# Kernel optimization log

Measured on AMD Instinct MI355X. Metric: run time of the kernel, lower is better.

The kernel has to match this reference:

```python
import jax, jax.numpy as jnp
import numpy as np

B, N, E = 8, 10000, 160000
T_IN, T_OUT, C_IN, C_OUT, HID = 12, 12, 2, 2, 128
FLAT = C_IN * T_IN  # 24
EPS = 1e-5  # BatchNorm1d default eps


def setup_inputs() -> dict:
    key = jax.random.key(0)
    ks = jax.random.split(key, 16)
    s = 0.05
    return {
        "x": jax.random.normal(ks[0], (B, T_IN, N, C_IN), jnp.float32),
        "edge_index": jax.random.randint(ks[1], (2, E), 0, N, dtype=jnp.int64),
        "Wl0": jax.random.normal(ks[2], (FLAT, HID), jnp.float32) * s,
        "Wr0": jax.random.normal(ks[3], (FLAT, HID), jnp.float32) * s,
        "bl0": jax.random.normal(ks[4], (HID,), jnp.float32) * s,
        "Wl12": jax.random.normal(ks[5], (2, HID, HID), jnp.float32) * s,
        "Wr12": jax.random.normal(ks[6], (2, HID, HID), jnp.float32) * s,
        "bl12": jax.random.normal(ks[7], (2, HID), jnp.float32) * s,
        "bn_g": jax.random.uniform(ks[8], (3, HID), jnp.float32, 0.5, 1.5),
        "bn_b": jax.random.normal(ks[9], (3, HID), jnp.float32) * s,
        "bn_m": jax.random.normal(ks[10], (3, HID), jnp.float32) * s,
        "bn_v": jax.random.uniform(ks[11], (3, HID), jnp.float32, 0.5, 1.5),
        "head_W": jax.random.normal(ks[12], (HID, T_OUT * C_OUT), jnp.float32) * s,
        "head_b": jax.random.normal(ks[13], (T_OUT * C_OUT,), jnp.float32) * s,
    }


def _sage_conv(h, src, dst, inv_deg, Wl, Wr, bl):
    # PyG SAGEConv (mean aggr): out = lin_l(mean_{j->i} x_j) + lin_r(x_i)
    msg = h[:, src, :]                                   # [B, E, F] gather
    agg = jnp.zeros_like(h).at[:, dst, :].add(msg)       # scatter-add
    mean = agg * inv_deg[None, :, None]                  # mean over neighbors
    return mean @ Wl + bl + h @ Wr


def reference(x, edge_index, Wl0, Wr0, bl0, Wl12, Wr12, bl12,
              bn_g, bn_b, bn_m, bn_v, head_W, head_b):
    src, dst = edge_index[0], edge_index[1]
    deg = jnp.zeros((N,), x.dtype).at[dst].add(1.0)
    inv_deg = 1.0 / jnp.maximum(deg, 1.0)

    # (B, T, N, C) -> (B, N, T*C)
    h = x.transpose(0, 2, 1, 3).reshape(B, N, FLAT)

    layers = [(Wl0, Wr0, bl0), (Wl12[0], Wr12[0], bl12[0]), (Wl12[1], Wr12[1], bl12[1])]
    for i, (Wl, Wr, bl) in enumerate(layers):
        h = _sage_conv(h, src, dst, inv_deg, Wl, Wr, bl)
        # BatchNorm1d in eval mode (running stats); Dropout is identity in eval
        h = (h - bn_m[i]) * (bn_g[i] / jnp.sqrt(bn_v[i] + EPS)) + bn_b[i]
        h = jax.nn.relu(h)

    out = h @ head_W + head_b                            # [B, N, T_out*C_out]
    out = out.reshape(B, N, T_OUT, C_OUT).transpose(0, 2, 1, 3)
    return out                                           # [B, T_out, N, C_out]
```

## Files before the change

kernel.cpp:

```cpp
#include <hip/hip_runtime.h>

#define NB 8
#define NNODE 10000
#define NEDGE 160000
#define MROWS 80000
#define TIN 12
#define EPSBN 1e-5f

typedef __attribute__((ext_vector_type(8))) short bf16x8;
typedef __attribute__((ext_vector_type(4))) float f32x4;
typedef unsigned short u16;
typedef unsigned int u32;

static __device__ __forceinline__ u16 f2bf(float f) {
    unsigned int u = __builtin_bit_cast(unsigned int, f);
    u = (u + 0x7fffu + ((u >> 16) & 1u)) >> 16;
    return (u16)u;
}
static __device__ __forceinline__ float bf2f(u16 h) {
    unsigned int u = ((unsigned int)h) << 16;
    return __builtin_bit_cast(float, u);
}

__global__ __launch_bounds__(256) void fused_pre(const float* __restrict__ x,
                                                 u16* __restrict__ X0,
                                                 const int* __restrict__ ei,
                                                 int* __restrict__ degi,
                                                 const float* __restrict__ Wl0,
                                                 const float* __restrict__ Wr0,
                                                 const float* __restrict__ bl0,
                                                 const float* __restrict__ Wl12,
                                                 const float* __restrict__ Wr12,
                                                 const float* __restrict__ bl12,
                                                 const float* __restrict__ g,
                                                 const float* __restrict__ bb,
                                                 const float* __restrict__ m,
                                                 const float* __restrict__ v,
                                                 u16* __restrict__ W0T, u16* __restrict__ W1T,
                                                 u16* __restrict__ W2T,
                                                 float* __restrict__ bias012) {
    int blk = blockIdx.x;
    if (blk < 3750) {
        int id = blk * 256 + threadIdx.x;
        if (id >= NB * TIN * NNODE) return;
        int n = id % NNODE;
        int bt = id / NNODE;
        int b = bt / TIN, tt = bt % TIN;
        float2 vv = *(const float2*)&x[(size_t)id * 2];
        u32 packed = (u32)f2bf(vv.x) | ((u32)f2bf(vv.y) << 16);
        *(u32*)&X0[(n * NB + b) * 64 + 24 + tt * 2] = packed;
    } else if (blk < 4375) {
        int e = (blk - 3750) * 256 + threadIdx.x;
        if (e < NEDGE) atomicAdd(&degi[ei[NEDGE + e]], 1);
    } else {
        int c = blk - 4375, k = threadIdx.x;
        float s0 = g[c] / sqrtf(v[c] + EPSBN);
        float s1 = g[128 + c] / sqrtf(v[128 + c] + EPSBN);
        float s2 = g[256 + c] / sqrtf(v[256 + c] + EPSBN);
        if (k < 64) {
            float val = (k < 24) ? Wl0[k * 128 + c] : ((k < 48) ? Wr0[(k - 24) * 128 + c] : 0.0f);
            W0T[c * 64 + k] = f2bf(val * s0);
        }
        float v1 = (k < 128) ? Wl12[k * 128 + c] : Wr12[(k - 128) * 128 + c];
        W1T[c * 256 + k] = f2bf(v1 * s1);
        float v2 = (k < 128) ? Wl12[128 * 128 + k * 128 + c]
                             : Wr12[128 * 128 + (k - 128) * 128 + c];
        W2T[c * 256 + k] = f2bf(v2 * s2);
        if (k < 3) {
            float sl = g[k * 128 + c] / sqrtf(v[k * 128 + c] + EPSBN);
            float blv = (k == 0) ? bl0[c] : bl12[(k - 1) * 128 + c];
            bias012[k * 128 + c] = blv * sl + bb[k * 128 + c] - m[k * 128 + c] * sl;
        }
    }
}

__global__ __launch_bounds__(1024) void scan_kernel(const int* __restrict__ degi,
                                                    int* __restrict__ row_ptr,
                                                    float* __restrict__ inv_deg,
                                                    int* __restrict__ cursor) {
    __shared__ int sdata[1024];
    const int t = threadIdx.x;
    const int CH = 10;
    const int i0 = t * CH;
    int sum = 0;
    for (int i = i0; i < i0 + CH && i < NNODE; ++i) sum += degi[i];
    sdata[t] = sum;
    for (int off = 1; off < 1024; off <<= 1) {
        __syncthreads();
        int vv = (t >= off) ? sdata[t - off] : 0;
        __syncthreads();
        sdata[t] += vv;
    }
    __syncthreads();
    int run = sdata[t] - sum;
    for (int i = i0; i < i0 + CH && i < NNODE; ++i) {
        row_ptr[i] = run;
        int d = degi[i];
        run += d;
        inv_deg[i] = 1.0f / (float)max(d, 1);
        cursor[i] = 0;
    }
    if (t == 1023) row_ptr[NNODE] = sdata[1023];
}

__global__ void csr_fill(const int* __restrict__ ei, const int* __restrict__ row_ptr,
                         int* __restrict__ cursor, int* __restrict__ csr_src) {
    int e = blockIdx.x * blockDim.x + threadIdx.x;
    if (e < NEDGE) {
        int d = ei[NEDGE + e];
        int pos = atomicAdd(&cursor[d], 1);
        csr_src[row_ptr[d] + pos] = ei[e];
    }
}

__global__ __launch_bounds__(192) void agg24(u16* __restrict__ X0,
                                             const int* __restrict__ rp,
                                             const int* __restrict__ cs,
                                             const float* __restrict__ inv) {
    int u = threadIdx.x;
    int n = blockIdx.x * 2 + (u / 96);
    int w = u % 96;
    int b = w / 12, cp = w % 12;
    int p0 = rp[n], p1 = rp[n + 1];
    float a0 = 0, a1 = 0, b0 = 0, b1 = 0, c0 = 0, c1 = 0, d0 = 0, d1 = 0;
    int p = p0;
    for (; p + 4 <= p1; p += 4) {
        int s0 = cs[p], s1 = cs[p + 1], s2 = cs[p + 2], s3 = cs[p + 3];
        u32 v0 = *(const u32*)&X0[(s0 * NB + b) * 64 + 24 + cp * 2];
        u32 v1 = *(const u32*)&X0[(s1 * NB + b) * 64 + 24 + cp * 2];
        u32 v2 = *(const u32*)&X0[(s2 * NB + b) * 64 + 24 + cp * 2];
        u32 v3 = *(const u32*)&X0[(s3 * NB + b) * 64 + 24 + cp * 2];
        a0 += bf2f((u16)(v0 & 0xffff)); a1 += bf2f((u16)(v0 >> 16));
        b0 += bf2f((u16)(v1 & 0xffff)); b1 += bf2f((u16)(v1 >> 16));
        c0 += bf2f((u16)(v2 & 0xffff)); c1 += bf2f((u16)(v2 >> 16));
        d0 += bf2f((u16)(v3 & 0xffff)); d1 += bf2f((u16)(v3 >> 16));
    }
    for (; p < p1; ++p) {
        int s = cs[p];
        u32 vv = *(const u32*)&X0[(s * NB + b) * 64 + 24 + cp * 2];
        a0 += bf2f((u16)(vv & 0xffff)); a1 += bf2f((u16)(vv >> 16));
    }
    float sc = inv[n];
    float r0 = (a0 + b0) + (c0 + d0), r1 = (a1 + b1) + (c1 + d1);
    u32 o = (u32)f2bf(r0 * sc) | ((u32)f2bf(r1 * sc) << 16);
    *(u32*)&X0[(n * NB + b) * 64 + cp * 2] = o;
}

__global__ __launch_bounds__(64) void agg128c(u16* __restrict__ X,
                                              const int* __restrict__ rp,
                                              const int* __restrict__ cs,
                                              const float* __restrict__ inv) {
    int bid = blockIdx.x;
    int c = bid & 7;
    int n = bid >> 3;
    int t = threadIdx.x;
    int b = t >> 3, q = t & 7;
    int p0 = rp[n], p1 = rp[n + 1];
    const u16* hb = X + ((size_t)(8 + c) * MROWS) * 16;
    float a0 = 0, a1 = 0, b0 = 0, b1 = 0, c0 = 0, c1 = 0, d0 = 0, d1 = 0;
    int p = p0;
    for (; p + 4 <= p1; p += 4) {
        int s0 = cs[p], s1 = cs[p + 1], s2 = cs[p + 2], s3 = cs[p + 3];
        u32 v0 = *(const u32*)&hb[(s0 * NB + b) * 16 + q * 2];
        u32 v1 = *(const u32*)&hb[(s1 * NB + b) * 16 + q * 2];
        u32 v2 = *(const u32*)&hb[(s2 * NB + b) * 16 + q * 2];
        u32 v3 = *(const u32*)&hb[(s3 * NB + b) * 16 + q * 2];
        a0 += bf2f((u16)(v0 & 0xffff)); a1 += bf2f((u16)(v0 >> 16));
        b0 += bf2f((u16)(v1 & 0xffff)); b1 += bf2f((u16)(v1 >> 16));
        c0 += bf2f((u16)(v2 & 0xffff)); c1 += bf2f((u16)(v2 >> 16));
        d0 += bf2f((u16)(v3 & 0xffff)); d1 += bf2f((u16)(v3 >> 16));
    }
    for (; p < p1; ++p) {
        int s = cs[p];
        u32 vv = *(const u32*)&hb[(s * NB + b) * 16 + q * 2];
        a0 += bf2f((u16)(vv & 0xffff)); a1 += bf2f((u16)(vv >> 16));
    }
    float sc = inv[n];
    float r0 = (a0 + b0) + (c0 + d0), r1 = (a1 + b1) + (c1 + d1);
    u32 o = (u32)f2bf(r0 * sc) | ((u32)f2bf(r1 * sc) << 16);
    *(u32*)&X[((size_t)c * MROWS + n * NB + b) * 16 + q * 2] = o;
}

#define LOADA(dst, stp) { \
    const int k0_ = (stp) * 32 + kg * 8; \
    _Pragma("unroll") \
    for (int m_ = 0; m_ < 4; ++m_) { \
        const int row_ = rowbase + m_ * 16; \
        const u16* ap_; \
        if (INC) ap_ = A + ((size_t)(k0_ >> 4) * MROWS + row_) * 16 + (k0_ & 15); \
        else     ap_ = A + (size_t)row_ * K + k0_; \
        dst[m_] = *(const bf16x8*)ap_; \
    } }

#define MFMAS(av, stp) { \
    const int k0_ = (stp) * 32 + kg * 8; \
    bf16x8 bv_[4]; \
    _Pragma("unroll") \
    for (int n_ = 0; n_ < 4; ++n_) \
        bv_[n_] = *(const bf16x8*)&Bs[wc * 64 + n_ * 16 + r16][k0_]; \
    _Pragma("unroll") \
    for (int m_ = 0; m_ < 4; ++m_) \
        _Pragma("unroll") \
        for (int n_ = 0; n_ < 4; ++n_) \
            acc[m_][n_] = __builtin_amdgcn_mfma_f32_16x16x32_bf16(av[m_], bv_[n_], acc[m_][n_], 0, 0, 0); }

template<int K, bool INC, bool OUTC>
__global__ __launch_bounds__(640) void gemm_mfma(const u16* __restrict__ A,
                                                 const u16* __restrict__ WT,
                                                 const float* __restrict__ bias,
                                                 u16* __restrict__ out) {
    constexpr int NSTEP = K / 32;
    __shared__ __align__(16) short Bs[128][K + 8];
    const int t = threadIdx.x;
    const int row0 = blockIdx.x * 320;
    const int lane = t & 63, wid = t >> 6;
    const int wr = wid >> 1, wc = wid & 1;
    const int r16 = lane & 15, kg = lane >> 4;

    if (t < 512) {
        const int col = t >> 2, k0 = (t & 3) * (K / 4);
        #pragma unroll
        for (int j = 0; j < K / 32; ++j)
            *(bf16x8*)&Bs[col][k0 + j * 8] =
                *(const bf16x8*)&WT[col * K + k0 + j * 8];
    }
    __syncthreads();

    f32x4 acc[4][4];
    #pragma unroll
    for (int m = 0; m < 4; ++m)
        #pragma unroll
        for (int n = 0; n < 4; ++n)
            acc[m][n] = (f32x4){0.f, 0.f, 0.f, 0.f};

    const int rowbase = row0 + wr * 64 + r16;

    bf16x8 avA[4], avB[4];
    LOADA(avA, 0)
    #pragma unroll
    for (int s2 = 0; s2 < NSTEP; s2 += 2) {
        if (s2 + 1 < NSTEP) LOADA(avB, s2 + 1)
        MFMAS(avA, s2)
        if (s2 + 2 < NSTEP) LOADA(avA, s2 + 2)
        if (s2 + 1 < NSTEP) MFMAS(avB, s2 + 1)
    }

    #pragma unroll
    for (int m = 0; m < 4; ++m) {
        #pragma unroll
        for (int n = 0; n < 4; ++n) {
            int col = wc * 64 + n * 16 + r16;
            float bvf = bias[col];
            #pragma unroll
            for (int r = 0; r < 4; ++r) {
                int grow = row0 + wr * 64 + m * 16 + kg * 4 + r;
                float val = fmaxf(acc[m][n][r] + bvf, 0.0f);
                u16 h = f2bf(val);
                if (OUTC)
                    out[((size_t)(8 + wc * 4 + n) * MROWS + grow) * 16 + r16] = h;
                else
                    out[(size_t)grow * 128 + col] = h;
            }
        }
    }
}

__global__ __launch_bounds__(256) void head_kernel(const u16* __restrict__ H3,
                                                   const float* __restrict__ hW,
                                                   const float* __restrict__ hb,
                                                   float* __restrict__ out) {
    __shared__ float Ws[128 * 24];
    __shared__ float bs[24];
    int t = threadIdx.x;
    for (int i = t; i < 128 * 24; i += 256) Ws[i] = hW[i];
    if (t < 24) bs[t] = hb[t];
    __syncthreads();
    int row = blockIdx.x * 256 + t;
    if (row >= MROWS) return;
    float acc[24];
    #pragma unroll
    for (int c = 0; c < 24; ++c) acc[c] = bs[c];
    const u16* a = &H3[(size_t)row * 128];
    for (int kq = 0; kq < 16; ++kq) {
        bf16x8 raw = *(const bf16x8*)&a[kq * 8];
        #pragma unroll
        for (int j = 0; j < 8; ++j) {
            float av = bf2f((u16)raw[j]);
            #pragma unroll
            for (int c = 0; c < 24; ++c)
                acc[c] = fmaf(av, Ws[(kq * 8 + j) * 24 + c], acc[c]);
        }
    }
    int n = row >> 3, b = row & 7;
    #pragma unroll
    for (int tt = 0; tt < 12; ++tt) {
        float2 o;
        o.x = acc[tt * 2 + 0];
        o.y = acc[tt * 2 + 1];
        *(float2*)&out[((b * TIN + tt) * NNODE + n) * 2] = o;
    }
}

extern "C" void kernel_launch(void* const* d_in, const int* in_sizes, int n_in,
                              void* d_out, int out_size, void* d_ws, size_t ws_size,
                              hipStream_t stream) {
    const float* x      = (const float*)d_in[0];
    const int*   ei     = (const int*)d_in[1];
    const float* Wl0    = (const float*)d_in[2];
    const float* Wr0    = (const float*)d_in[3];
    const float* bl0    = (const float*)d_in[4];
    const float* Wl12   = (const float*)d_in[5];
    const float* Wr12   = (const float*)d_in[6];
    const float* bl12   = (const float*)d_in[7];
    const float* bn_g   = (const float*)d_in[8];
    const float* bn_b   = (const float*)d_in[9];
    const float* bn_m   = (const float*)d_in[10];
    const float* bn_v   = (const float*)d_in[11];
    const float* headW  = (const float*)d_in[12];
    const float* headb  = (const float*)d_in[13];
    float* out = (float*)d_out;

    u16* X0 = (u16*)d_ws;
    u16* X1 = X0 + (size_t)MROWS * 64;
    u16* X2 = X1 + (size_t)MROWS * 256;
    u16* W0T = X2 + (size_t)MROWS * 256;
    u16* W1T = W0T + 128 * 64;
    u16* W2T = W1T + 128 * 256;
    float* bias012 = (float*)(W2T + 128 * 256);
    float* inv_deg = bias012 + 3 * 128;
    int* degi    = (int*)(inv_deg + NNODE);
    int* row_ptr = degi + NNODE;
    int* cursor  = row_ptr + (NNODE + 1);
    int* csr_src = cursor + NNODE;
    u16* H3 = X1;

    hipMemsetAsync(degi, 0, sizeof(int) * NNODE, stream);

    fused_pre<<<4503, 256, 0, stream>>>(x, X0, ei, degi, Wl0, Wr0, bl0, Wl12, Wr12,
                                        bl12, bn_g, bn_b, bn_m, bn_v,
                                        W0T, W1T, W2T, bias012);
    scan_kernel<<<1, 1024, 0, stream>>>(degi, row_ptr, inv_deg, cursor);
    csr_fill<<<(NEDGE + 255) / 256, 256, 0, stream>>>(ei, row_ptr, cursor, csr_src);

    agg24<<<NNODE / 2, 192, 0, stream>>>(X0, row_ptr, csr_src, inv_deg);
    gemm_mfma<64, false, true><<<250, 640, 0, stream>>>(X0, W0T, bias012, X1);
    agg128c<<<NNODE * 8, 64, 0, stream>>>(X1, row_ptr, csr_src, inv_deg);
    gemm_mfma<256, true, true><<<250, 640, 0, stream>>>(X1, W1T, bias012 + 128, X2);
    agg128c<<<NNODE * 8, 64, 0, stream>>>(X2, row_ptr, csr_src, inv_deg);
    gemm_mfma<256, true, false><<<250, 640, 0, stream>>>(X2, W2T, bias012 + 256, H3);
    head_kernel<<<(MROWS + 255) / 256, 256, 0, stream>>>(H3, headW, headb, out);
}
```

Before: 283.1 us.

## Fuse output head into last SAGE GEMM and shrink X0 row stride

The separate head kernel is folded into the epilogue of the third MFMA GEMM. The post-ReLU tile is staged in shared memory and each pair of threads computes 12 of the 24 head outputs per row, so the H3 intermediate is no longer written to and re-read from global memory, and one launch disappears. The first-layer buffer X0 now uses a 48-element row stride instead of 64. The input transpose now has one thread per row, packing all 12 timesteps into vector stores. The GEMM still reads K=64 with the smaller stride, so it relies on zero weight padding and a small tail pad past the last row. The fused epilogue also needs much more shared memory.

```diff
diff --git a/kernel.cpp b/kernel.cpp
--- a/kernel.cpp
+++ b/kernel.cpp
@@ -40,20 +40,25 @@
                                                  u16* __restrict__ W2T,
                                                  float* __restrict__ bias012) {
     int blk = blockIdx.x;
-    if (blk < 3750) {
-        int id = blk * 256 + threadIdx.x;
-        if (id >= NB * TIN * NNODE) return;
-        int n = id % NNODE;
-        int bt = id / NNODE;
-        int b = bt / TIN, tt = bt % TIN;
-        float2 vv = *(const float2*)&x[(size_t)id * 2];
-        u32 packed = (u32)f2bf(vv.x) | ((u32)f2bf(vv.y) << 16);
-        *(u32*)&X0[(n * NB + b) * 64 + 24 + tt * 2] = packed;
-    } else if (blk < 4375) {
-        int e = (blk - 3750) * 256 + threadIdx.x;
+    if (blk < 313) {
+        int row = blk * 256 + threadIdx.x;
+        if (row >= MROWS) return;
+        int n = row >> 3, b = row & 7;
+        u32 w[12];
+        #pragma unroll
+        for (int tt = 0; tt < 12; ++tt) {
+            float2 vv = *(const float2*)&x[(size_t)((b * 12 + tt) * NNODE + n) * 2];
+            w[tt] = (u32)f2bf(vv.x) | ((u32)f2bf(vv.y) << 16);
+        }
+        u32* dst = (u32*)&X0[(size_t)row * 48 + 24];
+        *(uint4*)(dst + 0) = make_uint4(w[0], w[1], w[2], w[3]);
+        *(uint4*)(dst + 4) = make_uint4(w[4], w[5], w[6], w[7]);
+        *(uint4*)(dst + 8) = make_uint4(w[8], w[9], w[10], w[11]);
+    } else if (blk < 938) {
+        int e = (blk - 313) * 256 + threadIdx.x;
         if (e < NEDGE) atomicAdd(&degi[ei[NEDGE + e]], 1);
     } else {
-        int c = blk - 4375, k = threadIdx.x;
+        int c = blk - 938, k = threadIdx.x;
         float s0 = g[c] / sqrtf(v[c] + EPSBN);
         float s1 = g[128 + c] / sqrtf(v[128 + c] + EPSBN);
         float s2 = g[256 + c] / sqrtf(v[256 + c] + EPSBN);
@@ -126,10 +131,10 @@
     int p = p0;
     for (; p + 4 <= p1; p += 4) {
         int s0 = cs[p], s1 = cs[p + 1], s2 = cs[p + 2], s3 = cs[p + 3];
-        u32 v0 = *(const u32*)&X0[(s0 * NB + b) * 64 + 24 + cp * 2];
-        u32 v1 = *(const u32*)&X0[(s1 * NB + b) * 64 + 24 + cp * 2];
-        u32 v2 = *(const u32*)&X0[(s2 * NB + b) * 64 + 24 + cp * 2];
-        u32 v3 = *(const u32*)&X0[(s3 * NB + b) * 64 + 24 + cp * 2];
+        u32 v0 = *(const u32*)&X0[(s0 * NB + b) * 48 + 24 + cp * 2];
+        u32 v1 = *(const u32*)&X0[(s1 * NB + b) * 48 + 24 + cp * 2];
+        u32 v2 = *(const u32*)&X0[(s2 * NB + b) * 48 + 24 + cp * 2];
+        u32 v3 = *(const u32*)&X0[(s3 * NB + b) * 48 + 24 + cp * 2];
         a0 += bf2f((u16)(v0 & 0xffff)); a1 += bf2f((u16)(v0 >> 16));
         b0 += bf2f((u16)(v1 & 0xffff)); b1 += bf2f((u16)(v1 >> 16));
         c0 += bf2f((u16)(v2 & 0xffff)); c1 += bf2f((u16)(v2 >> 16));
@@ -137,13 +142,13 @@
     }
     for (; p < p1; ++p) {
         int s = cs[p];
-        u32 vv = *(const u32*)&X0[(s * NB + b) * 64 + 24 + cp * 2];
+        u32 vv = *(const u32*)&X0[(s * NB + b) * 48 + 24 + cp * 2];
         a0 += bf2f((u16)(vv & 0xffff)); a1 += bf2f((u16)(vv >> 16));
     }
     float sc = inv[n];
     float r0 = (a0 + b0) + (c0 + d0), r1 = (a1 + b1) + (c1 + d1);
     u32 o = (u32)f2bf(r0 * sc) | ((u32)f2bf(r1 * sc) << 16);
-    *(u32*)&X0[(n * NB + b) * 64 + cp * 2] = o;
+    *(u32*)&X0[(n * NB + b) * 48 + cp * 2] = o;
 }
 
 __global__ __launch_bounds__(64) void agg128c(u16* __restrict__ X,
@@ -188,7 +193,7 @@
         const int row_ = rowbase + m_ * 16; \
         const u16* ap_; \
         if (INC) ap_ = A + ((size_t)(k0_ >> 4) * MROWS + row_) * 16 + (k0_ & 15); \
-        else     ap_ = A + (size_t)row_ * K + k0_; \
+        else     ap_ = A + (size_t)row_ * LDA + k0_; \
         dst[m_] = *(const bf16x8*)ap_; \
     } }
 
@@ -204,19 +209,34 @@
         for (int n_ = 0; n_ < 4; ++n_) \
             acc[m_][n_] = __builtin_amdgcn_mfma_f32_16x16x32_bf16(av[m_], bv_[n_], acc[m_][n_], 0, 0, 0); }
 
-template<int K, bool INC, bool OUTC>
+template<int K, int LDA, bool INC, bool HEAD>
 __global__ __launch_bounds__(640) void gemm_mfma(const u16* __restrict__ A,
                                                  const u16* __restrict__ WT,
                                                  const float* __restrict__ bias,
-                                                 u16* __restrict__ out) {
+                                                 const float* __restrict__ hW,
+                                                 const float* __restrict__ hb,
+                                                 u16* __restrict__ outc,
+                                                 float* __restrict__ outf) {
     constexpr int NSTEP = K / 32;
-    __shared__ __align__(16) short Bs[128][K + 8];
+    constexpr int BS_BYTES = 128 * (K + 8) * 2;
+    constexpr int HS_BYTES = 320 * 132 * 2;
+    constexpr int SMEM_BYTES = HEAD ? (HS_BYTES + 128 * 24 * 4 + 128) : BS_BYTES;
+    __shared__ __align__(16) char smem[SMEM_BYTES];
+    typedef short (*BsT)[K + 8];
+    BsT Bs = (BsT)smem;
+
     const int t = threadIdx.x;
     const int row0 = blockIdx.x * 320;
     const int lane = t & 63, wid = t >> 6;
     const int wr = wid >> 1, wc = wid & 1;
     const int r16 = lane & 15, kg = lane >> 4;
 
+    float* Wsf = (float*)(smem + HS_BYTES);
+    float* bsh = Wsf + 128 * 24;
+    if (HEAD) {
+        for (int i = t; i < 128 * 24; i += 640) Wsf[i] = hW[i];
+        if (t < 24) bsh[t] = hb[t];
+    }
     if (t < 512) {
         const int col = t >> 2, k0 = (t & 3) * (K / 4);
         #pragma unroll
@@ -245,59 +265,64 @@
         if (s2 + 1 < NSTEP) MFMAS(avB, s2 + 1)
     }
 
-    #pragma unroll
-    for (int m = 0; m < 4; ++m) {
-        #pragma unroll
-        for (int n = 0; n < 4; ++n) {
-            int col = wc * 64 + n * 16 + r16;
-            float bvf = bias[col];
+    if (!HEAD) {
+        #pragma unroll
+        for (int m = 0; m < 4; ++m)
             #pragma unroll
-            for (int r = 0; r < 4; ++r) {
-                int grow = row0 + wr * 64 + m * 16 + kg * 4 + r;
-                float val = fmaxf(acc[m][n][r] + bvf, 0.0f);
-                u16 h = f2bf(val);
-                if (OUTC)
-                    out[((size_t)(8 + wc * 4 + n) * MROWS + grow) * 16 + r16] = h;
-                else
-                    out[(size_t)grow * 128 + col] = h;
+            for (int n = 0; n < 4; ++n) {
+                int col = wc * 64 + n * 16 + r16;
+                float bvf = bias[col];
+                #pragma unroll
+                for (int r = 0; r < 4; ++r) {
+                    int grow = row0 + wr * 64 + m * 16 + kg * 4 + r;
+                    float val = fmaxf(acc[m][n][r] + bvf, 0.0f);
+                    outc[((size_t)(8 + wc * 4 + n) * MROWS + grow) * 16 + r16] = f2bf(val);
+                }
             }
-        }
-    }
-}
-
-__global__ __launch_bounds__(256) void head_kernel(const u16* __restrict__ H3,
-                                                   const float* __restrict__ hW,
-                                                   const float* __restrict__ hb,
-                                                   float* __restrict__ out) {
-    __shared__ float Ws[128 * 24];
-    __shared__ float bs[24];
-    int t = threadIdx.x;
-    for (int i = t; i < 128 * 24; i += 256) Ws[i] = hW[i];
-    if (t < 24) bs[t] = hb[t];
-    __syncthreads();
-    int row = blockIdx.x * 256 + t;
-    if (row >= MROWS) return;
-    float acc[24];
-    #pragma unroll
-    for (int c = 0; c < 24; ++c) acc[c] = bs[c];
-    const u16* a = &H3[(size_t)row * 128];
-    for (int kq = 0; kq < 16; ++kq) {
-        bf16x8 raw = *(const bf16x8*)&a[kq * 8];
-        #pragma unroll
-        for (int j = 0; j < 8; ++j) {
-            float av = bf2f((u16)raw[j]);
+    } else {
+        __syncthreads();
+        u16* Hs = (u16*)smem;
+        #pragma unroll
+        for (int m = 0; m < 4; ++m)
             #pragma unroll
-            for (int c = 0; c < 24; ++c)
-                acc[c] = fmaf(av, Ws[(kq * 8 + j) * 24 + c], acc[c]);
-        }
-    }
-    int n = row >> 3, b = row & 7;
-    #pragma unroll
-    for (int tt = 0; tt < 12; ++tt) {
-        float2 o;
-        o.x = acc[tt * 2 + 0];
-        o.y = acc[tt * 2 + 1];
-        *(float2*)&out[((b * TIN + tt) * NNODE + n) * 2] = o;
+            for (int n = 0; n < 4; ++n) {
+                int col = wc * 64 + n * 16 + r16;
+                float bvf = bias[col];
+                #pragma unroll
+                for (int r = 0; r < 4; ++r) {
+                    int lrow = wr * 64 + m * 16 + kg * 4 + r;
+                    Hs[lrow * 132 + col] = f2bf(fmaxf(acc[m][n][r] + bvf, 0.0f));
+                }
+            }
+        __syncthreads();
+        int lrow = t >> 1, half = t & 1;
+        const u32* hrow = (const u32*)(Hs + lrow * 132);
+        const float* wbase = Wsf + half * 12;
+        float a24[12];
+        #pragma unroll
+        for (int j = 0; j < 12; ++j) a24[j] = bsh[half * 12 + j];
+        #pragma unroll 4
+        for (int kq = 0; kq < 64; ++kq) {
+            u32 wv = hrow[kq];
+            float f0 = bf2f((u16)(wv & 0xffff));
+            float f1 = bf2f((u16)(wv >> 16));
+            const float* w0 = wbase + (kq * 2) * 24;
+            #pragma unroll
+            for (int j = 0; j < 12; ++j)
+                a24[j] = fmaf(f0, w0[j], a24[j]);
+            const float* w1 = wbase + (kq * 2 + 1) * 24;
+            #pragma unroll
+            for (int j = 0; j < 12; ++j)
+                a24[j] = fmaf(f1, w1[j], a24[j]);
+        }
+        int grow = row0 + lrow;
+        int n = grow >> 3, b = grow & 7;
+        #pragma unroll
+        for (int jj = 0; jj < 12; jj += 2) {
+            int tt = (half * 12 + jj) >> 1;
+            float2 o = {a24[jj], a24[jj + 1]};
+            *(float2*)&outf[((size_t)(b * TIN + tt) * NNODE + n) * 2] = o;
+        }
     }
 }
 
@@ -321,7 +346,7 @@
     float* out = (float*)d_out;
 
     u16* X0 = (u16*)d_ws;
-    u16* X1 = X0 + (size_t)MROWS * 64;
+    u16* X1 = X0 + (size_t)MROWS * 48 + 32;
     u16* X2 = X1 + (size_t)MROWS * 256;
     u16* W0T = X2 + (size_t)MROWS * 256;
     u16* W1T = W0T + 128 * 64;
@@ -332,21 +357,22 @@
     int* row_ptr = degi + NNODE;
     int* cursor  = row_ptr + (NNODE + 1);
     int* csr_src = cursor + NNODE;
-    u16* H3 = X1;
 
     hipMemsetAsync(degi, 0, sizeof(int) * NNODE, stream);
 
-    fused_pre<<<4503, 256, 0, stream>>>(x, X0, ei, degi, Wl0, Wr0, bl0, Wl12, Wr12,
+    fused_pre<<<1066, 256, 0, stream>>>(x, X0, ei, degi, Wl0, Wr0, bl0, Wl12, Wr12,
                                         bl12, bn_g, bn_b, bn_m, bn_v,
                                         W0T, W1T, W2T, bias012);
     scan_kernel<<<1, 1024, 0, stream>>>(degi, row_ptr, inv_deg, cursor);
     csr_fill<<<(NEDGE + 255) / 256, 256, 0, stream>>>(ei, row_ptr, cursor, csr_src);
 
     agg24<<<NNODE / 2, 192, 0, stream>>>(X0, row_ptr, csr_src, inv_deg);
-    gemm_mfma<64, false, true><<<250, 640, 0, stream>>>(X0, W0T, bias012, X1);
+    gemm_mfma<64, 48, false, false><<<250, 640, 0, stream>>>(X0, W0T, bias012,
+                                                             nullptr, nullptr, X1, nullptr);
     agg128c<<<NNODE * 8, 64, 0, stream>>>(X1, row_ptr, csr_src, inv_deg);
-    gemm_mfma<256, true, true><<<250, 640, 0, stream>>>(X1, W1T, bias012 + 128, X2);
+    gemm_mfma<256, 0, true, false><<<250, 640, 0, stream>>>(X1, W1T, bias012 + 128,
+                                                            nullptr, nullptr, X2, nullptr);
     agg128c<<<NNODE * 8, 64, 0, stream>>>(X2, row_ptr, csr_src, inv_deg);
-    gemm_mfma<256, true, false><<<250, 640, 0, stream>>>(X2, W2T, bias012 + 256, H3);
-    head_kernel<<<(MROWS + 255) / 256, 256, 0, stream>>>(H3, headW, headb, out);
-}
+    gemm_mfma<256, 0, true, true><<<250, 640, 0, stream>>>(X2, W2T, bias012 + 256,
+                                                           headW, headb, nullptr, out);
+}
```

Measured after the change: 248.5 us. 12.2% less time.
